# Performance work log

Hardware: AMD Instinct MI355X
Metric: run time of the kernel (lower is better)

## Reference

```python
import jax, jax.numpy as jnp
import numpy as np

DIM = 1024
NUM_HEADS = 16
HEAD_DIM = DIM // NUM_HEADS


def setup_inputs() -> dict:
    key = jax.random.key(0)
    k1, k2, k3, k4, k5 = jax.random.split(key, 5)
    B, N, C = 8, 1024, DIM
    x = jax.random.normal(k1, (B, N, C), dtype=jnp.float32)
    s_in = 1.0 / np.sqrt(C)
    w_qkv = jax.random.normal(k2, (C, 3 * C), dtype=jnp.float32) * s_in
    b_qkv = jnp.zeros((3 * C,), dtype=jnp.float32)
    w_proj = jax.random.normal(k3, (C, C), dtype=jnp.float32) * s_in
    b_proj = jnp.zeros((C,), dtype=jnp.float32)
    return {"x": x, "w_qkv": w_qkv, "b_qkv": b_qkv, "w_proj": w_proj, "b_proj": b_proj}


def reference(x, w_qkv, b_qkv, w_proj, b_proj):
    B, N, C = x.shape
    H, D = NUM_HEADS, C // NUM_HEADS
    scale = jnp.float32(1.0) / jnp.sqrt(jnp.float32(D))
    qkv = x @ w_qkv + b_qkv                      # [B, N, 3C]
    qkv = qkv.reshape(B, N, 3, H, D)
    qkv = jnp.transpose(qkv, (2, 0, 3, 1, 4))     # [3, B, H, N, D]
    q, k, v = qkv[0], qkv[1], qkv[2]
    attn = jnp.einsum('bhnd,bhmd->bhnm', q, k) * scale  # [B, H, N, N]
    attn = jax.nn.softmax(attn, axis=-1)
    out = jnp.einsum('bhnm,bhmd->bhnd', attn, v)  # [B, H, N, D]
    out = jnp.transpose(out, (0, 2, 1, 3)).reshape(B, N, C)
    return out @ w_proj + b_proj
```

## Files before the change

### kernel.cpp

```cpp
#include <hip/hip_runtime.h>
#include <stdint.h>
#include <stddef.h>


#define DEVI __device__ __forceinline__

typedef float f32x4 __attribute__((ext_vector_type(4)));
typedef float f32x16 __attribute__((ext_vector_type(16)));
typedef __bf16 bf16x8 __attribute__((ext_vector_type(8)));
typedef unsigned short u16x8 __attribute__((ext_vector_type(8)));
typedef unsigned short u16x4 __attribute__((ext_vector_type(4)));
typedef unsigned int u32;
typedef unsigned int u32x4 __attribute__((ext_vector_type(4)));

static constexpr int M1 = 8192;

DEVI unsigned short f2bf(float f) {
  uint32_t u = __builtin_bit_cast(uint32_t, f);
  u += 0x7FFFu + ((u >> 16) & 1u);
  return (unsigned short)(u >> 16);
}

DEVI float fexp2(float x) {
  float r;
  asm("v_exp_f32 %0, %1" : "=v"(r) : "v"(x));
  return r;
}

DEVI u32 cvtpk(float lo, float hi) {
  u32 r;
  asm("v_cvt_pk_bf16_f32 %0, %1, %2" : "=v"(r) : "v"(lo), "v"(hi));
  return r;
}

DEVI void plswap(u32& a, u32& b) {
  asm("v_permlane32_swap_b32 %0, %1" : "+v"(a), "+v"(b));
}

DEVI void gll16(const unsigned short* g, unsigned short* lds) {
  __builtin_amdgcn_global_load_lds(
      (const __attribute__((address_space(1))) void*)g,
      (__attribute__((address_space(3))) void*)lds, 16, 0, 0);
}

DEVI bf16x8 lds_frag(const unsigned short* p) {
  return __builtin_bit_cast(bf16x8, *(const u16x8*)p);
}

__global__ void k_cvt(const float* __restrict__ in, unsigned short* __restrict__ out, int n4) {
  int i = blockIdx.x * blockDim.x + threadIdx.x;
  if (i < n4) {
    float4 v = reinterpret_cast<const float4*>(in)[i];
    u16x4 o = { f2bf(v.x), f2bf(v.y), f2bf(v.z), f2bf(v.w) };
    reinterpret_cast<u16x4*>(out)[i] = o;
  }
}

__global__ void k_tr_cvt(const float* __restrict__ in, unsigned short* __restrict__ out,
                         int R, int Cc) {
  __shared__ float tile[32][33];
  int c0 = blockIdx.x * 32, r0 = blockIdx.y * 32;
  int tx = threadIdx.x, ty = threadIdx.y;
#pragma unroll
  for (int j = 0; j < 32; j += 8)
    tile[ty + j][tx] = in[(size_t)(r0 + ty + j) * Cc + c0 + tx];
  __syncthreads();
#pragma unroll
  for (int j = 0; j < 32; j += 8)
    out[(size_t)(c0 + ty + j) * R + r0 + tx] = f2bf(tile[tx][ty + j]);
}

__global__ void k_tr_v(const unsigned short* __restrict__ in, unsigned short* __restrict__ out) {
  __shared__ unsigned short t[32][33];
  int d0 = blockIdx.x * 32, n0 = blockIdx.y * 32, bh = blockIdx.z;
  const unsigned short* ip = in + (size_t)bh * 1024 * 64;
  unsigned short* op = out + (size_t)bh * 64 * 1024;
  int tx = threadIdx.x, ty = threadIdx.y;
#pragma unroll
  for (int j = 0; j < 32; j += 8)
    t[ty + j][tx] = ip[(size_t)(n0 + ty + j) * 64 + d0 + tx];
  __syncthreads();
#pragma unroll
  for (int j = 0; j < 32; j += 8)
    op[(size_t)(d0 + ty + j) * 1024 + n0 + tx] = t[tx][ty + j];
}

__global__ __launch_bounds__(512, 2)
void k_gemm1(const unsigned short* __restrict__ A,
             const unsigned short* __restrict__ Bt,
             const float* __restrict__ bias,
             unsigned short* __restrict__ Qp,
             unsigned short* __restrict__ Kp,
             unsigned short* __restrict__ Vp) {
  constexpr int K = 1024, NT = K / 64;
  __shared__ unsigned short As[2 * 256 * 64];
  __shared__ unsigned short Bs[2 * 256 * 64];

  const int tid = threadIdx.x;
  const int w = tid >> 6, l = tid & 63;
  const int ln = l & 15, kg = l >> 4;
  const int wr = w >> 2, wc = w & 3;

  const int bid = blockIdx.x;
  const int swz = (bid & 7) * 48 + (bid >> 3);
  const int rt = swz & 31, ct = swz >> 5;
  const int row0 = rt * 256, col0 = ct * 256;

  const unsigned short* Ag = A + (size_t)row0 * K;
  const unsigned short* Bg = Bt + (size_t)col0 * K;

  auto stageA = [&](int kt, int hf) {
    unsigned short* lb = &As[((kt & 1) * 256 + hf * 128) * 64];
#pragma unroll
    for (int j = 0; j < 2; j++) {
      int idx = j * 512 + tid;
      int r = idx >> 3, c = idx & 7;
      gll16(Ag + (size_t)(hf * 128 + r) * K + kt * 64 + ((c ^ (r & 7)) * 8), lb + idx * 8);
    }
  };
  auto stageB = [&](int kt, int hf) {
    unsigned short* lb = &Bs[((kt & 1) * 256 + hf * 128) * 64];
#pragma unroll
    for (int j = 0; j < 2; j++) {
      int idx = j * 512 + tid;
      int r = idx >> 3, c = idx & 7;
      gll16(Bg + (size_t)(hf * 128 + r) * K + kt * 64 + ((c ^ (r & 7)) * 8), lb + idx * 8);
    }
  };

  f32x4 acc[8][4] = {};
  bf16x8 am[4][2], b0[2][2], b1[2][2];

  stageA(0, 0); stageA(0, 1); stageB(0, 0); stageB(0, 1);
  stageA(1, 0); stageB(1, 0); stageB(1, 1);
  asm volatile("s_waitcnt vmcnt(6)" ::: "memory");
  __builtin_amdgcn_s_barrier();

  for (int T = 0; T < NT; T++) {
    const int dbase = (T & 1) * 256 * 64;

#pragma unroll
    for (int mi = 0; mi < 4; mi++)
#pragma unroll
      for (int kk = 0; kk < 2; kk++) {
        int r = wr * 128 + mi * 16 + ln;
        int c = (kk * 4 + kg) ^ (r & 7);
        am[mi][kk] = lds_frag(&As[dbase + r * 64 + c * 8]);
      }
#pragma unroll
    for (int ni = 0; ni < 2; ni++)
#pragma unroll
      for (int kk = 0; kk < 2; kk++) {
        int r = wc * 64 + ni * 16 + ln;
        int c = (kk * 4 + kg) ^ (r & 7);
        b0[ni][kk] = lds_frag(&Bs[dbase + r * 64 + c * 8]);
      }
    if (T + 1 < NT) stageA(T + 1, 1);
    __builtin_amdgcn_s_barrier();
    asm volatile("s_waitcnt lgkmcnt(0)" ::: "memory");
    __builtin_amdgcn_sched_barrier(0);
    __builtin_amdgcn_s_setprio(1);
#pragma unroll
    for (int mi = 0; mi < 4; mi++)
#pragma unroll
      for (int ni = 0; ni < 2; ni++)
#pragma unroll
        for (int kk = 0; kk < 2; kk++)
          acc[mi][ni] = __builtin_amdgcn_mfma_f32_16x16x32_bf16(am[mi][kk], b0[ni][kk], acc[mi][ni], 0, 0, 0);
    __builtin_amdgcn_s_setprio(0);
    __builtin_amdgcn_s_barrier();

#pragma unroll
    for (int ni = 0; ni < 2; ni++)
#pragma unroll
      for (int kk = 0; kk < 2; kk++) {
        int r = wc * 64 + (2 + ni) * 16 + ln;
        int c = (kk * 4 + kg) ^ (r & 7);
        b1[ni][kk] = lds_frag(&Bs[dbase + r * 64 + c * 8]);
      }
    __builtin_amdgcn_s_barrier();
    asm volatile("s_waitcnt lgkmcnt(0)" ::: "memory");
    __builtin_amdgcn_sched_barrier(0);
    __builtin_amdgcn_s_setprio(1);
#pragma unroll
    for (int mi = 0; mi < 4; mi++)
#pragma unroll
      for (int ni = 0; ni < 2; ni++)
#pragma unroll
        for (int kk = 0; kk < 2; kk++)
          acc[mi][2 + ni] = __builtin_amdgcn_mfma_f32_16x16x32_bf16(am[mi][kk], b1[ni][kk], acc[mi][2 + ni], 0, 0, 0);
    __builtin_amdgcn_s_setprio(0);
    __builtin_amdgcn_s_barrier();

#pragma unroll
    for (int mi = 0; mi < 4; mi++)
#pragma unroll
      for (int kk = 0; kk < 2; kk++) {
        int r = wr * 128 + (4 + mi) * 16 + ln;
        int c = (kk * 4 + kg) ^ (r & 7);
        am[mi][kk] = lds_frag(&As[dbase + r * 64 + c * 8]);
      }
    if (T + 2 < NT) stageB(T + 2, 0);
    __builtin_amdgcn_s_barrier();
    asm volatile("s_waitcnt lgkmcnt(0)" ::: "memory");
    __builtin_amdgcn_sched_barrier(0);
    __builtin_amdgcn_s_setprio(1);
#pragma unroll
    for (int mi = 0; mi < 4; mi++)
#pragma unroll
      for (int ni = 0; ni < 2; ni++)
#pragma unroll
        for (int kk = 0; kk < 2; kk++)
          acc[4 + mi][2 + ni] = __builtin_amdgcn_mfma_f32_16x16x32_bf16(am[mi][kk], b1[ni][kk], acc[4 + mi][2 + ni], 0, 0, 0);
    __builtin_amdgcn_s_setprio(0);
    __builtin_amdgcn_s_barrier();

    if (T + 2 < NT) { stageB(T + 2, 1); stageA(T + 2, 0); }
    __builtin_amdgcn_s_barrier();
    __builtin_amdgcn_s_setprio(1);
#pragma unroll
    for (int mi = 0; mi < 4; mi++)
#pragma unroll
      for (int ni = 0; ni < 2; ni++)
#pragma unroll
        for (int kk = 0; kk < 2; kk++)
          acc[4 + mi][ni] = __builtin_amdgcn_mfma_f32_16x16x32_bf16(am[mi][kk], b0[ni][kk], acc[4 + mi][ni], 0, 0, 0);
    __builtin_amdgcn_s_setprio(0);
    if (T + 2 < NT)      asm volatile("s_waitcnt vmcnt(6)" ::: "memory");
    else if (T + 1 < NT) asm volatile("s_waitcnt vmcnt(0)" ::: "memory");
    __builtin_amdgcn_s_barrier();
  }

  constexpr float QS = 0.18033688011112042f;
  const int three = col0 >> 10;
  const int hh = ((col0 & 1023) >> 6) + wc;
  unsigned short* tgt = (three == 0) ? Qp : (three == 1) ? Kp : Vp;
  const float sc = (three == 0) ? QS : 1.f;
  float bv[4];
#pragma unroll
  for (int n = 0; n < 4; n++) bv[n] = bias[col0 + wc * 64 + n * 16 + ln];
#pragma unroll
  for (int m = 0; m < 8; m++)
#pragma unroll
    for (int r = 0; r < 4; r++) {
      int row = row0 + wr * 128 + m * 16 + kg * 4 + r;
      int bb = row >> 10, nn = row & 1023;
      size_t base = ((size_t)(bb * 16 + hh) * 1024 + nn) * 64;
#pragma unroll
      for (int n = 0; n < 4; n++)
        tgt[base + n * 16 + ln] = f2bf((acc[m][n][r] + bv[n]) * sc);
    }
}

template <int EPI, int NCOLS>
__global__ __launch_bounds__(256, 2)
void k_gemm(const unsigned short* __restrict__ A,
            const unsigned short* __restrict__ Bt,
            const float* __restrict__ bias,
            float* __restrict__ Out) {
  constexpr int K = 1024, NK = K / 32;
  __shared__ unsigned short As[2][128 * 32];
  __shared__ unsigned short Bs[2][128 * 32];

  const int tid = threadIdx.x;
  const int w = tid >> 6, l = tid & 63;
  const int ln = l & 15, kg = l >> 4;
  const int wr = w >> 1, wc = w & 1;

  const int rt = blockIdx.x % (M1 / 128);
  const int ct = blockIdx.x / (M1 / 128);
  const int row0 = rt * 128, col0 = ct * 128;

  f32x4 acc[4][4] = {};

  const unsigned short* Ag = A + (size_t)row0 * K;
  const unsigned short* Bg = Bt + (size_t)col0 * K;

  auto stage = [&](int buf, int kt) {
    const unsigned short* ga = Ag + kt * 32;
    const unsigned short* gb = Bg + kt * 32;
#pragma unroll
    for (int j = 0; j < 2; j++) {
      int c = j * 256 + w * 64 + l;
      int r = c >> 2, s = c & 3;
      int ss = s ^ ((r >> 1) & 3);
      gll16(ga + (size_t)r * K + ss * 8, &As[buf][(j * 256 + w * 64) * 8]);
      gll16(gb + (size_t)r * K + ss * 8, &Bs[buf][(j * 256 + w * 64) * 8]);
    }
  };

  stage(0, 0);
  __syncthreads();

  int buf = 0;
  for (int kt = 0; kt < NK; kt++) {
    if (kt + 1 < NK) stage(buf ^ 1, kt + 1);

    bf16x8 af[4], bfr[4];
#pragma unroll
    for (int m = 0; m < 4; m++) {
      int r = wr * 64 + m * 16 + ln;
      int sl = kg ^ ((r >> 1) & 3);
      af[m] = lds_frag(&As[buf][r * 32 + sl * 8]);
    }
#pragma unroll
    for (int n = 0; n < 4; n++) {
      int r = wc * 64 + n * 16 + ln;
      int sl = kg ^ ((r >> 1) & 3);
      bfr[n] = lds_frag(&Bs[buf][r * 32 + sl * 8]);
    }
    __builtin_amdgcn_s_setprio(1);
#pragma unroll
    for (int m = 0; m < 4; m++)
#pragma unroll
      for (int n = 0; n < 4; n++)
        acc[m][n] = __builtin_amdgcn_mfma_f32_16x16x32_bf16(af[m], bfr[n], acc[m][n], 0, 0, 0);
    __builtin_amdgcn_s_setprio(0);

    __syncthreads();
    buf ^= 1;
  }

  float bv[4];
#pragma unroll
  for (int n = 0; n < 4; n++) bv[n] = bias[col0 + wc * 64 + n * 16 + ln];
#pragma unroll
  for (int m = 0; m < 4; m++)
#pragma unroll
    for (int r = 0; r < 4; r++) {
      int row = row0 + wr * 64 + m * 16 + kg * 4 + r;
#pragma unroll
      for (int n = 0; n < 4; n++)
        Out[(size_t)row * 1024 + col0 + wc * 64 + n * 16 + ln] = acc[m][n][r] + bv[n];
    }
}

__global__ __launch_bounds__(256, 4)
void k_attn(const unsigned short* __restrict__ Qg, const unsigned short* __restrict__ Kg,
            const unsigned short* __restrict__ Vtg, unsigned short* __restrict__ AO) {
  __shared__ unsigned short Ks[2][64 * 64];
  __shared__ unsigned short Vs[2][64 * 64];

  const int tid = threadIdx.x;
  const int w = tid >> 6, l = tid & 63;
  const int lq = l & 31, b = l >> 5;

  const int bh = blockIdx.x;
  const int qt = blockIdx.y;
  const int qbase = qt * 128 + w * 32;

  bf16x8 qf[4];
#pragma unroll
  for (int kk = 0; kk < 4; kk++) {
    size_t off = ((size_t)bh * 1024 + qbase + lq) * 64 + kk * 16 + b * 8;
    qf[kk] = __builtin_bit_cast(bf16x8, *(const u16x8*)(Qg + off));
  }

  f32x16 acc[2] = {};
  float mrun = -1e30f, lrun = 0.f;

  const unsigned short* Kbh = Kg + (size_t)bh * 1024 * 64;
  const unsigned short* Vbh = Vtg + (size_t)bh * 64 * 1024;

  auto stage = [&](int buf, int t) {
#pragma unroll
    for (int j = 0; j < 2; j++) {
      int c = j * 256 + w * 64 + l;
      int r = c >> 3, s = c & 7;
      int ss = s ^ (r & 7);
      gll16(Kbh + (size_t)(t * 64 + r) * 64 + ss * 8, &Ks[buf][(j * 256 + w * 64) * 8]);
      gll16(Vbh + (size_t)r * 1024 + t * 64 + ss * 8, &Vs[buf][(j * 256 + w * 64) * 8]);
    }
  };

  stage(0, 0);
  __syncthreads();

  int buf = 0;
  for (int t = 0; t < 16; t++) {
    if (t + 1 < 16) stage(buf ^ 1, t + 1);

    f32x16 s[2];
    __builtin_amdgcn_s_setprio(1);
#pragma unroll
    for (int kb = 0; kb < 2; kb++) {
      f32x16 z = {};
#pragma unroll
      for (int kk = 0; kk < 4; kk++) {
        int row = kb * 32 + lq;
        int ss = (kk * 2 + b) ^ (row & 7);
        bf16x8 kf = lds_frag(&Ks[buf][row * 64 + ss * 8]);
        z = __builtin_amdgcn_mfma_f32_32x32x16_bf16(kf, qf[kk], z, 0, 0, 0);
      }
      s[kb] = z;
    }
    __builtin_amdgcn_s_setprio(0);

    float tm = s[0][0];
#pragma unroll
    for (int kb = 0; kb < 2; kb++)
#pragma unroll
      for (int r = 0; r < 16; r++) tm = fmaxf(tm, s[kb][r]);
    tm = fmaxf(tm, __shfl_xor(tm, 32));

    if (!__all(tm <= mrun + 8.f)) {
      float mnew = fmaxf(mrun, tm);
      float al = fexp2(mrun - mnew);
      mrun = mnew;
      lrun *= al;
#pragma unroll
      for (int r = 0; r < 16; r++) {
        float aq = __shfl(al, (r & 3) + 8 * (r >> 2) + 4 * b);
        acc[0][r] *= aq;
        acc[1][r] *= aq;
      }
    }

    float rs = 0.f;
#pragma unroll
    for (int kb = 0; kb < 2; kb++)
#pragma unroll
      for (int r = 0; r < 16; r++) {
        float pv = fexp2(s[kb][r] - mrun);
        s[kb][r] = pv;
        rs += pv;
      }
    rs += __shfl_xor(rs, 32);
    lrun += rs;

    bf16x8 pa[4];
#pragma unroll
    for (int kb = 0; kb < 2; kb++) {
      u32 pk[4][2];
#pragma unroll
      for (int t4 = 0; t4 < 4; t4++) {
        pk[t4][0] = cvtpk(s[kb][t4 * 4 + 0], s[kb][t4 * 4 + 1]);
        pk[t4][1] = cvtpk(s[kb][t4 * 4 + 2], s[kb][t4 * 4 + 3]);
      }
#pragma unroll
      for (int sh = 0; sh < 2; sh++) {
        u32 a0 = pk[2 * sh][0], b0 = pk[2 * sh + 1][0];
        plswap(a0, b0);
        u32 a1 = pk[2 * sh][1], b1 = pk[2 * sh + 1][1];
        plswap(a1, b1);
        u32x4 fr = { a0, a1, b0, b1 };
        pa[kb * 2 + sh] = __builtin_bit_cast(bf16x8, fr);
      }
    }

    __builtin_amdgcn_s_setprio(1);
#pragma unroll
    for (int n = 0; n < 2; n++) {
#pragma unroll
      for (int st = 0; st < 4; st++) {
        int row = n * 32 + lq;
        int ss = (st * 2 + b) ^ (row & 7);
        bf16x8 vb = lds_frag(&Vs[buf][row * 64 + ss * 8]);
        acc[n] = __builtin_amdgcn_mfma_f32_32x32x16_bf16(pa[st], vb, acc[n], 0, 0, 0);
      }
    }
    __builtin_amdgcn_s_setprio(0);

    __syncthreads();
    buf ^= 1;
  }

  const int bb = bh >> 4, h = bh & 15;
  float linv = 1.f / lrun;
#pragma unroll
  for (int r = 0; r < 16; r++) {
    float lq_r = __shfl(linv, (r & 3) + 8 * (r >> 2) + 4 * b);
    int row = qbase + (r & 3) + 8 * (r >> 2) + 4 * b;
    size_t base = ((size_t)(bb * 1024 + row)) * 1024 + h * 64;
#pragma unroll
    for (int n = 0; n < 2; n++)
      AO[base + n * 32 + lq] = f2bf(acc[n][r] * lq_r);
  }
}

extern "C" void kernel_launch(void* const* d_in, const int* in_sizes, int n_in,
                              void* d_out, int out_size, void* d_ws, size_t ws_size,
                              hipStream_t stream) {
  const float* x      = (const float*)d_in[0];
  const float* w_qkv  = (const float*)d_in[1];
  const float* b_qkv  = (const float*)d_in[2];
  const float* w_proj = (const float*)d_in[3];
  const float* b_proj = (const float*)d_in[4];
  float* out = (float*)d_out;

  constexpr size_t SZ_XB  = (size_t)8192 * 1024 * 2;
  constexpr size_t SZ_WQ  = (size_t)3072 * 1024 * 2;
  constexpr size_t SZ_WP  = (size_t)1024 * 1024 * 2;
  constexpr size_t SZ_QKV = (size_t)8 * 16 * 1024 * 64 * 2;
  char* ws = (char*)d_ws;
  unsigned short* xb     = (unsigned short*)(ws);
  unsigned short* wqkvT  = (unsigned short*)(ws + SZ_XB);
  unsigned short* wprojT = (unsigned short*)(ws + SZ_XB + SZ_WQ);
  unsigned short* Qb     = (unsigned short*)(ws + SZ_XB + SZ_WQ + SZ_WP);
  unsigned short* Kb     = (unsigned short*)(ws + SZ_XB + SZ_WQ + SZ_WP + SZ_QKV);
  unsigned short* Vtb    = (unsigned short*)(ws + SZ_XB + SZ_WQ + SZ_WP + 2 * SZ_QKV);
  unsigned short* VrawAO = (unsigned short*)(ws + SZ_XB + SZ_WQ + SZ_WP + 3 * SZ_QKV);
  size_t needed = SZ_XB + SZ_WQ + SZ_WP + 4 * SZ_QKV;
  if (ws_size < needed) return;

  k_cvt<<<8192, 256, 0, stream>>>(x, xb, 8192 * 1024 / 4);
  dim3 tb(32, 8);
  k_tr_cvt<<<dim3(96, 32), tb, 0, stream>>>(w_qkv, wqkvT, 1024, 3072);
  k_tr_cvt<<<dim3(32, 32), tb, 0, stream>>>(w_proj, wprojT, 1024, 1024);
  k_gemm1<<<384, 512, 0, stream>>>(xb, wqkvT, b_qkv, Qb, Kb, VrawAO);
  k_tr_v<<<dim3(2, 32, 128), tb, 0, stream>>>(VrawAO, Vtb);
  k_attn<<<dim3(128, 8), 256, 0, stream>>>(Qb, Kb, Vtb, VrawAO);
  k_gemm<2, 1024><<<64 * 8, 256, 0, stream>>>(VrawAO, wprojT, b_proj, out);
}
```

Measured before the change: 250.2 us.

## Prepack K/V into MFMA fragment order and load attention operands directly from global

Replaces the V transpose kernel with a pack kernel that rearranges K and V into per-lane MFMA fragment order, so the attention kernel reads each operand with one contiguous 16-byte global load per lane. Shared-memory staging, double buffering and the per-tile barriers in attention are removed. The QKV GEMM block-to-tile mapping is also changed so each XCD covers a compact block of tiles, aiming at better L2 reuse. The trade-off is that global-load latency is no longer hidden by asynchronous LDS prefetch, and each K/V tile is fetched by every wave through L2 rather than shared within the block.

```diff
diff --git a/kernel.cpp b/kernel.cpp
--- a/kernel.cpp
+++ b/kernel.cpp
@@ -47,6 +47,10 @@
   return __builtin_bit_cast(bf16x8, *(const u16x8*)p);
 }
 
+DEVI bf16x8 gfrag(const unsigned short* p) {
+  return __builtin_bit_cast(bf16x8, *(const u16x8*)p);
+}
+
 __global__ void k_cvt(const float* __restrict__ in, unsigned short* __restrict__ out, int n4) {
   int i = blockIdx.x * blockDim.x + threadIdx.x;
   if (i < n4) {
@@ -70,19 +74,39 @@
     out[(size_t)(c0 + ty + j) * R + r0 + tx] = f2bf(tile[tx][ty + j]);
 }
 
-__global__ void k_tr_v(const unsigned short* __restrict__ in, unsigned short* __restrict__ out) {
-  __shared__ unsigned short t[32][33];
-  int d0 = blockIdx.x * 32, n0 = blockIdx.y * 32, bh = blockIdx.z;
-  const unsigned short* ip = in + (size_t)bh * 1024 * 64;
-  unsigned short* op = out + (size_t)bh * 64 * 1024;
-  int tx = threadIdx.x, ty = threadIdx.y;
-#pragma unroll
-  for (int j = 0; j < 32; j += 8)
-    t[ty + j][tx] = ip[(size_t)(n0 + ty + j) * 64 + d0 + tx];
+__global__ __launch_bounds__(256)
+void k_pack(const unsigned short* __restrict__ K, const unsigned short* __restrict__ V,
+            unsigned short* __restrict__ Kpk, unsigned short* __restrict__ Vpk) {
+  __shared__ unsigned short vt[64][80];
+  const int t = blockIdx.x, bh = blockIdx.y;
+  const int tid = threadIdx.x, l = tid & 63, g = tid >> 6;
+  const int lq = l & 31, b = l >> 5;
+  const unsigned short* Kt = K + ((size_t)bh * 1024 + t * 64) * 64;
+  const unsigned short* Vt = V + ((size_t)bh * 1024 + t * 64) * 64;
+  unsigned short* Ko = Kpk + (((size_t)bh * 16 + t) * 8) * 512;
+  unsigned short* Vo = Vpk + (((size_t)bh * 16 + t) * 8) * 512;
+
+#pragma unroll
+  for (int j = 0; j < 2; j++) {
+    int idx = tid + j * 256;
+    int r = idx >> 3, c = (idx & 7) * 8;
+    *(u16x8*)&vt[r][c] = *(const u16x8*)&Vt[r * 64 + c];
+  }
+#pragma unroll
+  for (int j = 0; j < 2; j++) {
+    int f = g * 2 + j, kb = f >> 2, kk = f & 3;
+    u16x8 kv = *(const u16x8*)&Kt[(kb * 32 + lq) * 64 + kk * 16 + b * 8];
+    *(u16x8*)&Ko[f * 512 + l * 8] = kv;
+  }
   __syncthreads();
 #pragma unroll
-  for (int j = 0; j < 32; j += 8)
-    op[(size_t)(d0 + ty + j) * 1024 + n0 + tx] = t[tx][ty + j];
+  for (int j = 0; j < 2; j++) {
+    int f = g * 2 + j, n = f >> 2, st = f & 3;
+    u16x8 vv;
+#pragma unroll
+    for (int e = 0; e < 8; e++) vv[e] = vt[(st * 2 + b) * 8 + e][n * 32 + lq];
+    *(u16x8*)&Vo[f * 512 + l * 8] = vv;
+  }
 }
 
 __global__ __launch_bounds__(512, 2)
@@ -102,8 +126,9 @@
   const int wr = w >> 2, wc = w & 3;
 
   const int bid = blockIdx.x;
-  const int swz = (bid & 7) * 48 + (bid >> 3);
-  const int rt = swz & 31, ct = swz >> 5;
+  const int xcd = bid & 7, ii = bid >> 3;
+  const int rt = (xcd >> 1) * 8 + (ii & 7);
+  const int ct = (xcd & 1) * 6 + (ii >> 3);
   const int row0 = rt * 256, col0 = ct * 256;
 
   const unsigned short* Ag = A + (size_t)row0 * K;
@@ -336,11 +361,8 @@
 }
 
 __global__ __launch_bounds__(256, 4)
-void k_attn(const unsigned short* __restrict__ Qg, const unsigned short* __restrict__ Kg,
-            const unsigned short* __restrict__ Vtg, unsigned short* __restrict__ AO) {
-  __shared__ unsigned short Ks[2][64 * 64];
-  __shared__ unsigned short Vs[2][64 * 64];
-
+void k_attn(const unsigned short* __restrict__ Qg, const unsigned short* __restrict__ Kpk,
+            const unsigned short* __restrict__ Vpk, unsigned short* __restrict__ AO) {
   const int tid = threadIdx.x;
   const int w = tid >> 6, l = tid & 63;
   const int lq = l & 31, b = l >> 5;
@@ -353,32 +375,19 @@
 #pragma unroll
   for (int kk = 0; kk < 4; kk++) {
     size_t off = ((size_t)bh * 1024 + qbase + lq) * 64 + kk * 16 + b * 8;
-    qf[kk] = __builtin_bit_cast(bf16x8, *(const u16x8*)(Qg + off));
+    qf[kk] = gfrag(Qg + off);
   }
 
   f32x16 acc[2] = {};
   float mrun = -1e30f, lrun = 0.f;
 
-  const unsigned short* Kbh = Kg + (size_t)bh * 1024 * 64;
-  const unsigned short* Vbh = Vtg + (size_t)bh * 64 * 1024;
-
-  auto stage = [&](int buf, int t) {
-#pragma unroll
-    for (int j = 0; j < 2; j++) {
-      int c = j * 256 + w * 64 + l;
-      int r = c >> 3, s = c & 7;
-      int ss = s ^ (r & 7);
-      gll16(Kbh + (size_t)(t * 64 + r) * 64 + ss * 8, &Ks[buf][(j * 256 + w * 64) * 8]);
-      gll16(Vbh + (size_t)r * 1024 + t * 64 + ss * 8, &Vs[buf][(j * 256 + w * 64) * 8]);
-    }
-  };
-
-  stage(0, 0);
-  __syncthreads();
-
-  int buf = 0;
+  const unsigned short* Kp = Kpk + (size_t)bh * 16 * 8 * 512;
+  const unsigned short* Vp = Vpk + (size_t)bh * 16 * 8 * 512;
+
+#pragma unroll 1
   for (int t = 0; t < 16; t++) {
-    if (t + 1 < 16) stage(buf ^ 1, t + 1);
+    const unsigned short* Kt = Kp + (size_t)t * 8 * 512 + l * 8;
+    const unsigned short* Vt = Vp + (size_t)t * 8 * 512 + l * 8;
 
     f32x16 s[2];
     __builtin_amdgcn_s_setprio(1);
@@ -387,9 +396,7 @@
       f32x16 z = {};
 #pragma unroll
       for (int kk = 0; kk < 4; kk++) {
-        int row = kb * 32 + lq;
-        int ss = (kk * 2 + b) ^ (row & 7);
-        bf16x8 kf = lds_frag(&Ks[buf][row * 64 + ss * 8]);
+        bf16x8 kf = gfrag(Kt + (kb * 4 + kk) * 512);
         z = __builtin_amdgcn_mfma_f32_32x32x16_bf16(kf, qf[kk], z, 0, 0, 0);
       }
       s[kb] = z;
@@ -453,16 +460,11 @@
     for (int n = 0; n < 2; n++) {
 #pragma unroll
       for (int st = 0; st < 4; st++) {
-        int row = n * 32 + lq;
-        int ss = (st * 2 + b) ^ (row & 7);
-        bf16x8 vb = lds_frag(&Vs[buf][row * 64 + ss * 8]);
+        bf16x8 vb = gfrag(Vt + (n * 4 + st) * 512);
         acc[n] = __builtin_amdgcn_mfma_f32_32x32x16_bf16(pa[st], vb, acc[n], 0, 0, 0);
       }
     }
     __builtin_amdgcn_s_setprio(0);
-
-    __syncthreads();
-    buf ^= 1;
   }
 
   const int bb = bh >> 4, h = bh & 15;
@@ -498,8 +500,10 @@
   unsigned short* wprojT = (unsigned short*)(ws + SZ_XB + SZ_WQ);
   unsigned short* Qb     = (unsigned short*)(ws + SZ_XB + SZ_WQ + SZ_WP);
   unsigned short* Kb     = (unsigned short*)(ws + SZ_XB + SZ_WQ + SZ_WP + SZ_QKV);
-  unsigned short* Vtb    = (unsigned short*)(ws + SZ_XB + SZ_WQ + SZ_WP + 2 * SZ_QKV);
-  unsigned short* VrawAO = (unsigned short*)(ws + SZ_XB + SZ_WQ + SZ_WP + 3 * SZ_QKV);
+  unsigned short* Vraw   = (unsigned short*)(ws + SZ_XB + SZ_WQ + SZ_WP + 2 * SZ_QKV);
+  unsigned short* Vpk    = (unsigned short*)(ws + SZ_XB + SZ_WQ + SZ_WP + 3 * SZ_QKV);
+  unsigned short* Kpk    = xb;
+  unsigned short* AOb    = Kb;
   size_t needed = SZ_XB + SZ_WQ + SZ_WP + 4 * SZ_QKV;
   if (ws_size < needed) return;
 
@@ -507,8 +511,8 @@
   dim3 tb(32, 8);
   k_tr_cvt<<<dim3(96, 32), tb, 0, stream>>>(w_qkv, wqkvT, 1024, 3072);
   k_tr_cvt<<<dim3(32, 32), tb, 0, stream>>>(w_proj, wprojT, 1024, 1024);
-  k_gemm1<<<384, 512, 0, stream>>>(xb, wqkvT, b_qkv, Qb, Kb, VrawAO);
-  k_tr_v<<<dim3(2, 32, 128), tb, 0, stream>>>(VrawAO, Vtb);
-  k_attn<<<dim3(128, 8), 256, 0, stream>>>(Qb, Kb, Vtb, VrawAO);
-  k_gemm<2, 1024><<<64 * 8, 256, 0, stream>>>(VrawAO, wprojT, b_proj, out);
-}
+  k_gemm1<<<384, 512, 0, stream>>>(xb, wqkvT, b_qkv, Qb, Kb, Vraw);
+  k_pack<<<dim3(16, 128), 256, 0, stream>>>(Kb, Vraw, Kpk, Vpk);
+  k_attn<<<dim3(128, 8), 256, 0, stream>>>(Qb, Kpk, Vpk, AOb);
+  k_gemm<2, 1024><<<64 * 8, 256, 0, stream>>>(AOb, wprojT, b_proj, out);
+}
```

New measurement: 247.6 us. No clear change (-1.0%).
